# Optimization experiments

Hardware: AMD Instinct MI355X
Metric: run time of the kernel (lower is better)

The kernel has to match this reference:

```python
import jax, jax.numpy as jnp
import numpy as np

B, S, E, H = 4, 1024, 256, 8
D = E // H


def setup_inputs() -> dict:
    key = jax.random.key(0)
    ks = jax.random.split(key, 10)
    def lin(k, fin, fout):
        return jax.random.normal(k, (fin, fout), jnp.float32) / np.sqrt(fin)
    return {
        'x': jax.random.normal(ks[0], (B, S, E), jnp.float32),
        'Wq': lin(ks[1], E, E),
        'Wk': lin(ks[2], E, E),
        'Wv': lin(ks[3], E, E),
        'W_off1': lin(ks[4], E, E // 2),
        'b_off1': jnp.zeros((E // 2,), jnp.float32),
        'W_off2': lin(ks[5], E // 2, 2 * H),
        'b_off2': jnp.zeros((2 * H,), jnp.float32),
        'W_out': lin(ks[6], E, E),
        'b_out': jnp.zeros((E,), jnp.float32),
    }


def _forward(x, Wq, Wk, Wv, W_off1, b_off1, W_off2, b_off2, W_out, b_out):
    Bb, Ss, Ee = x.shape
    scale = 1.0 / np.sqrt(D)
    # offsets: (B,S,H,2) -- [...,0]=x-offset (col), [...,1]=y-offset (row)
    off = jax.nn.gelu(x @ W_off1 + b_off1, approximate=False) @ W_off2 + b_off2
    off = off.reshape(Bb, Ss, H, 2)
    q = (x @ Wq).reshape(Bb, Ss, H, D).transpose(0, 2, 1, 3)  # bhsd
    k = (x @ Wk).reshape(Bb, Ss, H, D).transpose(0, 2, 1, 3)
    v = (x @ Wv).reshape(Bb, Ss, H, D).transpose(0, 2, 1, 3)
    scores = jnp.einsum('bhid,bhjd->bhij', q, k) * scale  # (B,H,S,S)

    ox = off[..., 0].transpose(0, 2, 1)  # (B,H,S)
    oy = off[..., 1].transpose(0, 2, 1)
    cols = jnp.arange(Ss, dtype=x.dtype)
    xs = cols[None, None, None, :] + ox[..., None]          # (B,H,S,S) sample col
    ys = cols[None, None, :, None] + oy[..., None]          # (B,H,S,1) sample row

    x0 = jnp.floor(xs); x1 = x0 + 1.0
    y0 = jnp.floor(ys); y1 = y0 + 1.0
    wx = xs - x0  # (B,H,S,S)
    wy = ys - y0  # (B,H,S,1)
    lim = jnp.asarray(Ss - 1, x.dtype)

    def corner(yf, xf):
        # bilinear corner sample with zeros padding (align_corners=True)
        yc = jnp.clip(yf, 0, lim).astype(jnp.int32)
        xc = jnp.clip(xf, 0, lim).astype(jnp.int32)
        rows = jnp.take_along_axis(scores, jnp.broadcast_to(yc, scores.shape), axis=2)
        vals = jnp.take_along_axis(rows, jnp.broadcast_to(xc, rows.shape), axis=3)
        valid = (yf >= 0) & (yf <= lim) & (xf >= 0) & (xf <= lim)
        return jnp.where(valid, vals, jnp.zeros((), x.dtype))

    deformed = (corner(y0, x0) * (1 - wy) * (1 - wx)
                + corner(y0, x1) * (1 - wy) * wx
                + corner(y1, x0) * wy * (1 - wx)
                + corner(y1, x1) * wy * wx)

    attn = jax.nn.softmax(deformed, axis=-1)  # dropout is identity in eval
    out = jnp.einsum('bhij,bhjd->bhid', attn, v)
    out = out.transpose(0, 2, 1, 3).reshape(Bb, Ss, Ee)
    return out @ W_out + b_out


def reference(x, Wq, Wk, Wv, W_off1, b_off1, W_off2, b_off2, W_out, b_out):
    return _forward(x, Wq, Wk, Wv, W_off1, b_off1, W_off2, b_off2, W_out, b_out)
```

## Files before the change

### kernel.cpp

```cpp
#include <hip/hip_runtime.h>

typedef unsigned short u16;
typedef __attribute__((ext_vector_type(8))) short short8;
typedef __attribute__((ext_vector_type(4))) float f32x4;

__device__ __forceinline__ float bf2f(u16 u) {
    union { unsigned int i; float f; } z;
    z.i = ((unsigned int)u) << 16;
    return z.f;
}
__device__ __forceinline__ u16 f2bf(float f) {
    union { float f; unsigned int i; } z;
    z.f = f;
    unsigned int i = z.i;
    return (u16)((i + 0x7fffu + ((i >> 16) & 1u)) >> 16);
}
__device__ __forceinline__ int sniff_bf16(const u16* __restrict__ x) {
    u16 u = x[threadIdx.x & 63];
    int e = (u >> 7) & 0xFF;
    bool sane = (e >= 110 && e <= 135) || (u == 0);
    unsigned long long m = __ballot(sane);
    return (__popcll(m) >= 50) ? 1 : 0;
}
__device__ __forceinline__ float cvt_elem(const void* p, int i, int fl) {
    return fl ? bf2f(((const u16*)p)[i]) : ((const float*)p)[i];
}

#define SB 1024
#define EB 256
#define NH 8
#define HD 32

__global__ __launch_bounds__(256) void k_prep(
    const void* x, const void* wq, const void* wk, const void* wv, const void* w1,
    const void* w2, const void* wo, const void* b1, const void* b2, const void* bo,
    u16* __restrict__ xb, u16* __restrict__ Wcat, u16* __restrict__ Wot,
    u16* __restrict__ W2t, float* __restrict__ b1f, float* __restrict__ b2f,
    float* __restrict__ bof) {
    __shared__ float tile[64][65];
    int fl = sniff_bf16((const u16*)x);
    int t = threadIdx.x;
    int bid = blockIdx.x;
    if (bid < 1024) {
        int idx = bid * 1024 + t * 4;
        if (fl) {
            *(ushort4*)(xb + idx) = *(const ushort4*)((const u16*)x + idx);
        } else {
            float4 v = *(const float4*)((const float*)x + idx);
            ushort4 s;
            s.x = f2bf(v.x); s.y = f2bf(v.y); s.z = f2bf(v.z); s.w = f2bf(v.w);
            *(ushort4*)(xb + idx) = s;
        }
    } else if (bid == 1024) {
        #pragma unroll
        for (int it = 0; it < 10; ++it) {
            int idx = it * 256 + t;
            if (idx < 2048) {
                int n = idx >> 7, kk = idx & 127;
                W2t[idx] = f2bf(cvt_elem(w2, kk * 16 + n, fl));
            }
            else if (idx < 2176)  b1f[idx - 2048] = cvt_elem(b1, idx - 2048, fl);
            else if (idx < 2192)  b2f[idx - 2176] = cvt_elem(b2, idx - 2176, fl);
            else if (idx < 2448)  bof[idx - 2192] = cvt_elem(bo, idx - 2192, fl);
        }
    } else {
        int rel = bid - 1025;
        int z = rel >> 4, rr = rel & 15;
        int k0 = (rr & 3) * 64, n0 = (rr >> 2) * 64;
        const void* src;
        u16* dst;
        int ncols;
        if (z == 0)      { src = wq; dst = Wcat;             ncols = 256; }
        else if (z == 1) { src = wk; dst = Wcat + 256 * 256; ncols = 256; }
        else if (z == 2) { src = wv; dst = Wcat + 512 * 256; ncols = 256; }
        else if (z == 3) { src = w1; dst = Wcat + 768 * 256; ncols = 128; }
        else             { src = wo; dst = Wot;              ncols = 256; }
        if (n0 >= ncols) return;
        int lr = t >> 6, lc = t & 63;
        #pragma unroll
        for (int it = 0; it < 16; ++it) {
            int r = it * 4 + lr;
            tile[r][lc] = cvt_elem(src, (k0 + r) * ncols + n0 + lc, fl);
        }
        __syncthreads();
        #pragma unroll
        for (int it = 0; it < 16; ++it) {
            int n = it * 4 + lr;
            dst[(size_t)(n0 + n) * 256 + k0 + lc] = f2bf(tile[lc][n]);
        }
    }
}

__global__ __launch_bounds__(256) void k_qkvh(
    const u16* __restrict__ xb, const u16* __restrict__ Wt, const float* __restrict__ b1f,
    u16* __restrict__ q, u16* __restrict__ k, u16* __restrict__ v, u16* __restrict__ hb) {
    int t = threadIdx.x;
    int w = t >> 6, L = t & 63;
    int lane15 = L & 15, quad = L >> 4;
    int Wid = blockIdx.x * 4 + w;
    int mtile = Wid & 127, ntile = Wid >> 7;
    int m0 = mtile * 32, n0 = ntile * 32;
    const u16* ap0 = xb + (size_t)(m0 + lane15) * 256 + quad * 8;
    const u16* ap1 = ap0 + 16 * 256;
    const u16* bp0 = Wt + (size_t)(n0 + lane15) * 256 + quad * 8;
    const u16* bp1 = bp0 + 16 * 256;
    bool vreg = (ntile >= 16 && ntile < 24);
    f32x4 acc[2][2];
    #pragma unroll
    for (int a = 0; a < 2; ++a)
        #pragma unroll
        for (int c = 0; c < 2; ++c) acc[a][c] = (f32x4){0.0f, 0.0f, 0.0f, 0.0f};
    if (!vreg) {
        #pragma unroll
        for (int kc = 0; kc < 256; kc += 32) {
            short8 a0 = *(const short8*)(ap0 + kc);
            short8 a1 = *(const short8*)(ap1 + kc);
            short8 b0 = *(const short8*)(bp0 + kc);
            short8 b1 = *(const short8*)(bp1 + kc);
            acc[0][0] = __builtin_amdgcn_mfma_f32_16x16x32_bf16(b0, a0, acc[0][0], 0, 0, 0);
            acc[0][1] = __builtin_amdgcn_mfma_f32_16x16x32_bf16(b1, a0, acc[0][1], 0, 0, 0);
            acc[1][0] = __builtin_amdgcn_mfma_f32_16x16x32_bf16(b0, a1, acc[1][0], 0, 0, 0);
            acc[1][1] = __builtin_amdgcn_mfma_f32_16x16x32_bf16(b1, a1, acc[1][1], 0, 0, 0);
        }
    } else {
        #pragma unroll
        for (int kc = 0; kc < 256; kc += 32) {
            short8 a0 = *(const short8*)(ap0 + kc);
            short8 a1 = *(const short8*)(ap1 + kc);
            short8 b0 = *(const short8*)(bp0 + kc);
            short8 b1 = *(const short8*)(bp1 + kc);
            acc[0][0] = __builtin_amdgcn_mfma_f32_16x16x32_bf16(a0, b0, acc[0][0], 0, 0, 0);
            acc[0][1] = __builtin_amdgcn_mfma_f32_16x16x32_bf16(a0, b1, acc[0][1], 0, 0, 0);
            acc[1][0] = __builtin_amdgcn_mfma_f32_16x16x32_bf16(a1, b0, acc[1][0], 0, 0, 0);
            acc[1][1] = __builtin_amdgcn_mfma_f32_16x16x32_bf16(a1, b1, acc[1][1], 0, 0, 0);
        }
    }
    if (ntile < 16) {
        u16* dst = (ntile < 8) ? q : k;
        int hh = ntile & 7;
        #pragma unroll
        for (int xt = 0; xt < 2; ++xt)
            #pragma unroll
            for (int wt = 0; wt < 2; ++wt) {
                int m = m0 + xt * 16 + lane15;
                int b = m >> 10, s = m & 1023;
                int d = wt * 16 + quad * 4;
                ushort4 st;
                st.x = f2bf(acc[xt][wt][0]); st.y = f2bf(acc[xt][wt][1]);
                st.z = f2bf(acc[xt][wt][2]); st.w = f2bf(acc[xt][wt][3]);
                *(ushort4*)(dst + (((size_t)(b * NH + hh)) * SB + s) * HD + d) = st;
            }
    } else if (vreg) {
        int nl = (ntile - 16) * 32;
        #pragma unroll
        for (int mt = 0; mt < 2; ++mt)
            #pragma unroll
            for (int nt = 0; nt < 2; ++nt) {
                int n = nl + nt * 16 + lane15;
                int hh = n >> 5, d = n & 31;
                int mbase = m0 + mt * 16 + quad * 4;
                int b = mbase >> 10, s0 = mbase & 1023;
                ushort4 st;
                st.x = f2bf(acc[mt][nt][0]); st.y = f2bf(acc[mt][nt][1]);
                st.z = f2bf(acc[mt][nt][2]); st.w = f2bf(acc[mt][nt][3]);
                *(ushort4*)(v + (b * NH + hh) * (SB * HD) + (s0 >> 3) * 256 + d * 8 + (s0 & 7)) = st;
            }
    } else {
        int nl = (ntile - 24) * 32;
        #pragma unroll
        for (int xt = 0; xt < 2; ++xt)
            #pragma unroll
            for (int wt = 0; wt < 2; ++wt) {
                int m = m0 + xt * 16 + lane15;
                int hn = nl + wt * 16 + quad * 4;
                ushort4 st;
                #pragma unroll
                for (int reg = 0; reg < 4; ++reg) {
                    float aa = acc[xt][wt][reg] + b1f[hn + reg];
                    float g = 0.5f * aa * (1.0f + erff(aa * 0.70710678118654752f));
                    ((u16*)&st)[reg] = f2bf(g);
                }
                *(ushort4*)(hb + (size_t)m * 128 + hn) = st;
            }
    }
}

__global__ __launch_bounds__(256) void k_qprime(
    const u16* __restrict__ hb, const u16* __restrict__ W2t, const float* __restrict__ b2f,
    float2* __restrict__ prmA, float4* __restrict__ prmB) {
    int t = threadIdx.x;
    int w = t >> 6, L = t & 63;
    int lane15 = L & 15, quad = L >> 4;
    int m0 = (blockIdx.x * 4 + w) * 16;
    const u16* ap = hb + (size_t)(m0 + lane15) * 128 + quad * 8;
    const u16* bp = W2t + (size_t)lane15 * 128 + quad * 8;
    f32x4 acc = {0.0f, 0.0f, 0.0f, 0.0f};
    #pragma unroll
    for (int c = 0; c < 4; ++c) {
        short8 a = *(const short8*)(ap + c * 32);
        short8 bfr = *(const short8*)(bp + c * 32);
        acc = __builtin_amdgcn_mfma_f32_16x16x32_bf16(a, bfr, acc, 0, 0, 0);
    }
    const float scale = 0.17677669529663687f;
    int n = lane15, h = n >> 1;
    float bb = b2f[n];
    #pragma unroll
    for (int reg = 0; reg < 4; ++reg) {
        int m = m0 + quad * 4 + reg;
        int i = m & 1023;
        float val = acc[reg] + bb;
        if ((n & 1) == 0) {
            float fxf = floorf(val);
            float wx = val - fxf;
            fxf = fminf(fmaxf(fxf, -1028.0f), 1028.0f);
            prmA[m * 8 + h] = make_float2(fxf, wx);
        } else {
            float ysf = (float)i + val;
            float y0f = floorf(ysf);
            float wy = ysf - y0f;
            float y1f = y0f + 1.0f;
            float alA = scale * (1.0f - wy) * ((y0f >= 0.0f && y0f <= 1023.0f) ? 1.0f : 0.0f);
            float alB = scale * wy * ((y1f >= 0.0f && y1f <= 1023.0f) ? 1.0f : 0.0f);
            float yc0 = fminf(fmaxf(y0f, 0.0f), 1023.0f);
            float yc1 = fminf(fmaxf(y1f, 0.0f), 1023.0f);
            prmB[m * 8 + h] = make_float4(alA, alB, yc0, yc1);
        }
    }
}

#define TSTR 1056
#define BLEND4A(R)                                                    \
    _Pragma("unroll")                                                 \
    for (int jj = 0; jj < 4; ++jj) {                                  \
        float dd = wxm * A8[(R) + jj] + wx * A8[(R) + jj + 1];        \
        dv[c * 4 + jj] = dd;                                          \
        lmax = fmaxf(lmax, dd);                                       \
    }

__global__ __launch_bounds__(256) void k_attn(
    const u16* __restrict__ q, const u16* __restrict__ kmat,
    const float2* __restrict__ prmA, const float4* __restrict__ prmB,
    const u16* __restrict__ vfrag, u16* __restrict__ attn) {
    __shared__ u16 tbuf[16][TSTR];
    __shared__ float invLs[16];
    float* red = (float*)&tbuf[0][0];
    int t = threadIdx.x;
    int w = t >> 6, L = t & 63;
    int lane15 = L & 15, quad = L >> 4;
    int bh = blockIdx.y, it0 = blockIdx.x * 16;
    int b = bh >> 3, h = bh & 7;
    int mg0 = b * SB + it0;

    {
        int row = t >> 4, ii = t & 15;
        tbuf[row][ii] = 0;
        tbuf[row][1040 + ii] = 0;
    }

    const u16* qb = q + (size_t)bh * SB * HD;
    float4 pB = prmB[(size_t)(mg0 + lane15) * 8 + h];
    int yc0 = (int)pB.z, yc1 = (int)pB.w;
    short8 q0 = *(const short8*)(qb + yc0 * HD + quad * 8);
    short8 q1 = *(const short8*)(qb + yc1 * HD + quad * 8);
    union { short8 v; u16 a[8]; } afr;
    #pragma unroll
    for (int s = 0; s < 8; ++s)
        afr.a[s] = f2bf(pB.x * bf2f((u16)q0[s]) + pB.y * bf2f((u16)q1[s]));

    const u16* kb = kmat + (size_t)bh * SB * HD;
    int c0 = w * 256;
    #pragma unroll
    for (int nt = 0; nt < 16; ++nt) {
        short8 bk = *(const short8*)(kb + (size_t)(c0 + nt * 16 + lane15) * HD + quad * 8);
        f32x4 z = {0.0f, 0.0f, 0.0f, 0.0f};
        f32x4 acc = __builtin_amdgcn_mfma_f32_16x16x32_bf16(bk, afr.v, z, 0, 0, 0);
        uint2 pk;
        pk.x = (unsigned)f2bf(acc[0]) | ((unsigned)f2bf(acc[1]) << 16);
        pk.y = (unsigned)f2bf(acc[2]) | ((unsigned)f2bf(acc[3]) << 16);
        *(uint2*)&tbuf[lane15][16 + c0 + nt * 16 + quad * 4] = pk;
    }
    __syncthreads();

    #pragma unroll
    for (int r = 0; r < 4; ++r) {
        int m = w * 4 + r;
        float2 pA = prmA[(size_t)(mg0 + m) * 8 + h];
        int fx = (int)pA.x;
        float wx = pA.y, wxm = 1.0f - wx;
        int qd = fx >> 2, rm = fx & 3;
        float dv[16];
        float lmax = -3.0e38f;
        #pragma unroll
        for (int c = 0; c < 4; ++c) {
            int colbase = c * 256 + 4 * (qd + L);
            int rd = colbase < -16 ? -16 : (colbase > 1032 ? 1032 : colbase);
            const u16* rp = &tbuf[m][16 + rd];
            ushort4 lo = *(const ushort4*)rp;
            ushort4 hi = *(const ushort4*)(rp + 4);
            float A8[8];
            A8[0] = bf2f(lo.x); A8[1] = bf2f(lo.y); A8[2] = bf2f(lo.z); A8[3] = bf2f(lo.w);
            A8[4] = bf2f(hi.x); A8[5] = bf2f(hi.y); A8[6] = bf2f(hi.z); A8[7] = bf2f(hi.w);
            if (rm == 0) { BLEND4A(0) }
            else if (rm == 1) { BLEND4A(1) }
            else if (rm == 2) { BLEND4A(2) }
            else { BLEND4A(3) }
        }
        #pragma unroll
        for (int o = 1; o < 64; o <<= 1) lmax = fmaxf(lmax, __shfl_xor(lmax, o));
        float ls = 0.0f;
        #pragma unroll
        for (int z = 0; z < 16; ++z) { dv[z] = __expf(dv[z] - lmax); ls += dv[z]; }
        #pragma unroll
        for (int o = 1; o < 64; o <<= 1) ls += __shfl_xor(ls, o);
        #pragma unroll
        for (int c = 0; c < 4; ++c) {
            unsigned lo = (unsigned)f2bf(dv[c * 4 + 0]) | ((unsigned)f2bf(dv[c * 4 + 1]) << 16);
            unsigned hi = (unsigned)f2bf(dv[c * 4 + 2]) | ((unsigned)f2bf(dv[c * 4 + 3]) << 16);
            *(uint2*)&tbuf[m][16 + c * 256 + 4 * L] = make_uint2(lo, hi);
        }
        if (L == 0) invLs[m] = 1.0f / ls;
    }
    __syncthreads();

    const u16* vb = vfrag + bh * (SB * HD);
    f32x4 acc0 = {0.0f, 0.0f, 0.0f, 0.0f};
    f32x4 acc1 = {0.0f, 0.0f, 0.0f, 0.0f};
    int kc0 = w * 256;
    #pragma unroll
    for (int c = 0; c < 8; ++c) {
        int kc = kc0 + c * 32;
        short8 a = *(const short8*)&tbuf[lane15][16 + kc + quad * 8];
        const u16* bp = vb + ((kc >> 3) + quad) * (HD * 8);
        short8 b0 = *(const short8*)(bp + lane15 * 8);
        short8 b1 = *(const short8*)(bp + (lane15 + 16) * 8);
        acc0 = __builtin_amdgcn_mfma_f32_16x16x32_bf16(a, b0, acc0, 0, 0, 0);
        acc1 = __builtin_amdgcn_mfma_f32_16x16x32_bf16(a, b1, acc1, 0, 0, 0);
    }
    __syncthreads();
    *(f32x4*)&red[(((size_t)w * 2 + 0) * 64 + L) * 4] = acc0;
    *(f32x4*)&red[(((size_t)w * 2 + 1) * 64 + L) * 4] = acc1;
    __syncthreads();
    {
        int row = t >> 4, col = t & 15;
        int lsrc = col + 16 * (row >> 2);
        int reg = row & 3;
        float s0 = red[((0 * 64 + lsrc)) * 4 + reg] + red[((2 * 64 + lsrc)) * 4 + reg]
                 + red[((4 * 64 + lsrc)) * 4 + reg] + red[((6 * 64 + lsrc)) * 4 + reg];
        float s1 = red[((1 * 64 + lsrc)) * 4 + reg] + red[((3 * 64 + lsrc)) * 4 + reg]
                 + red[((5 * 64 + lsrc)) * 4 + reg] + red[((7 * 64 + lsrc)) * 4 + reg];
        float il = invLs[row];
        size_t o = ((size_t)(b * SB + it0 + row)) * EB + h * HD;
        attn[o + col]      = f2bf(s0 * il);
        attn[o + 16 + col] = f2bf(s1 * il);
    }
}

__global__ __launch_bounds__(256) void k_out(
    const u16* __restrict__ a, const u16* __restrict__ Wot, const float* __restrict__ bof,
    const u16* __restrict__ xsniff, void* __restrict__ outp) {
    int fl = sniff_bf16(xsniff);
    int t = threadIdx.x;
    int w = t >> 6, L = t & 63;
    int lane15 = L & 15, quad = L >> 4;
    int Wid = blockIdx.x * 4 + w;
    int m0 = (Wid & 255) * 16, n0 = (Wid >> 8) * 32;
    const u16* ap  = a + (size_t)(m0 + lane15) * 256 + quad * 8;
    const u16* bp0 = Wot + (size_t)(n0 + lane15) * 256 + quad * 8;
    const u16* bp1 = bp0 + 16 * 256;
    f32x4 acc0 = {0.0f, 0.0f, 0.0f, 0.0f};
    f32x4 acc1 = {0.0f, 0.0f, 0.0f, 0.0f};
    #pragma unroll
    for (int kc = 0; kc < 256; kc += 32) {
        short8 av = *(const short8*)(ap + kc);
        short8 b0 = *(const short8*)(bp0 + kc);
        short8 b1 = *(const short8*)(bp1 + kc);
        acc0 = __builtin_amdgcn_mfma_f32_16x16x32_bf16(b0, av, acc0, 0, 0, 0);
        acc1 = __builtin_amdgcn_mfma_f32_16x16x32_bf16(b1, av, acc1, 0, 0, 0);
    }
    int m = m0 + lane15;
    #pragma unroll
    for (int wt = 0; wt < 2; ++wt) {
        const f32x4& ac = wt ? acc1 : acc0;
        int n = n0 + wt * 16 + quad * 4;
        float4 bz = *(const float4*)(bof + n);
        float v0 = ac[0] + bz.x, v1 = ac[1] + bz.y, v2 = ac[2] + bz.z, v3 = ac[3] + bz.w;
        if (fl) {
            ushort4 st;
            st.x = f2bf(v0); st.y = f2bf(v1); st.z = f2bf(v2); st.w = f2bf(v3);
            *(ushort4*)((u16*)outp + (size_t)m * 256 + n) = st;
        } else {
            *(float4*)((float*)outp + (size_t)m * 256 + n) = make_float4(v0, v1, v2, v3);
        }
    }
}

extern "C" void kernel_launch(void* const* d_in, const int* in_sizes, int n_in,
                              void* d_out, int out_size, void* d_ws, size_t ws_size,
                              hipStream_t stream) {
    char* ws = (char*)d_ws;
    u16*    xb   = (u16*)(ws);
    u16*    Wcat = (u16*)(ws + 2097152);
    u16*    Wot  = (u16*)(ws + 2555904);
    u16*    W2t  = (u16*)(ws + 2686976);
    float*  b1f  = (float*)(ws + 2691072);
    float*  b2f  = (float*)(ws + 2691584);
    float*  bof  = (float*)(ws + 2691648);
    u16*    q    = (u16*)(ws + 2692672);
    u16*    k    = (u16*)(ws + 4789824);
    u16*    v    = (u16*)(ws + 6886976);
    u16*    hb   = (u16*)(ws + 8984128);
    u16*    attn = (u16*)(ws + 10032704);
    float2* prmA = (float2*)(ws + 12129856);
    float4* prmB = (float4*)(ws + 12392000);

    hipLaunchKernelGGL(k_prep, dim3(1105), dim3(256), 0, stream,
                       d_in[0], d_in[1], d_in[2], d_in[3], d_in[4],
                       d_in[6], d_in[8], d_in[5], d_in[7], d_in[9],
                       xb, Wcat, Wot, W2t, b1f, b2f, bof);
    hipLaunchKernelGGL(k_qkvh, dim3(896), dim3(256), 0, stream, xb, Wcat, b1f, q, k, v, hb);
    hipLaunchKernelGGL(k_qprime, dim3(64), dim3(256), 0, stream, hb, W2t, b2f, prmA, prmB);
    hipLaunchKernelGGL(k_attn, dim3(64, 32), dim3(256), 0, stream, q, k, prmA, prmB, v, attn);
    hipLaunchKernelGGL(k_out, dim3(512), dim3(256), 0, stream, attn, Wot, bof,
                       (const u16*)d_in[0], (u16*)d_out);
}
```

Measured before the change: 147.9 us.

## Fuse offset projection into attention kernel and drop the qprime launch

Removes the separate k_qprime kernel and recomputes the second offset MLP layer inside k_attn with one small MFMA per wave. The x/y offsets are extracted with lane shuffles. This removes one kernel launch and the prmA/prmB round trip through global memory. In exchange, every attention block (across all heads) recomputes the 16x16 offset tile redundantly. It also changes the shared tile row stride from 1056 to 1064, which may affect LDS bank conflicts.

```diff
diff --git a/kernel.cpp b/kernel.cpp
--- a/kernel.cpp
+++ b/kernel.cpp
@@ -185,50 +185,7 @@
     }
 }
 
-__global__ __launch_bounds__(256) void k_qprime(
-    const u16* __restrict__ hb, const u16* __restrict__ W2t, const float* __restrict__ b2f,
-    float2* __restrict__ prmA, float4* __restrict__ prmB) {
-    int t = threadIdx.x;
-    int w = t >> 6, L = t & 63;
-    int lane15 = L & 15, quad = L >> 4;
-    int m0 = (blockIdx.x * 4 + w) * 16;
-    const u16* ap = hb + (size_t)(m0 + lane15) * 128 + quad * 8;
-    const u16* bp = W2t + (size_t)lane15 * 128 + quad * 8;
-    f32x4 acc = {0.0f, 0.0f, 0.0f, 0.0f};
-    #pragma unroll
-    for (int c = 0; c < 4; ++c) {
-        short8 a = *(const short8*)(ap + c * 32);
-        short8 bfr = *(const short8*)(bp + c * 32);
-        acc = __builtin_amdgcn_mfma_f32_16x16x32_bf16(a, bfr, acc, 0, 0, 0);
-    }
-    const float scale = 0.17677669529663687f;
-    int n = lane15, h = n >> 1;
-    float bb = b2f[n];
-    #pragma unroll
-    for (int reg = 0; reg < 4; ++reg) {
-        int m = m0 + quad * 4 + reg;
-        int i = m & 1023;
-        float val = acc[reg] + bb;
-        if ((n & 1) == 0) {
-            float fxf = floorf(val);
-            float wx = val - fxf;
-            fxf = fminf(fmaxf(fxf, -1028.0f), 1028.0f);
-            prmA[m * 8 + h] = make_float2(fxf, wx);
-        } else {
-            float ysf = (float)i + val;
-            float y0f = floorf(ysf);
-            float wy = ysf - y0f;
-            float y1f = y0f + 1.0f;
-            float alA = scale * (1.0f - wy) * ((y0f >= 0.0f && y0f <= 1023.0f) ? 1.0f : 0.0f);
-            float alB = scale * wy * ((y1f >= 0.0f && y1f <= 1023.0f) ? 1.0f : 0.0f);
-            float yc0 = fminf(fmaxf(y0f, 0.0f), 1023.0f);
-            float yc1 = fminf(fmaxf(y1f, 0.0f), 1023.0f);
-            prmB[m * 8 + h] = make_float4(alA, alB, yc0, yc1);
-        }
-    }
-}
-
-#define TSTR 1056
+#define TSTR 1064
 #define BLEND4A(R)                                                    \
     _Pragma("unroll")                                                 \
     for (int jj = 0; jj < 4; ++jj) {                                  \
@@ -239,7 +196,8 @@
 
 __global__ __launch_bounds__(256) void k_attn(
     const u16* __restrict__ q, const u16* __restrict__ kmat,
-    const float2* __restrict__ prmA, const float4* __restrict__ prmB,
+    const u16* __restrict__ hb, const u16* __restrict__ W2t,
+    const float* __restrict__ b2f,
     const u16* __restrict__ vfrag, u16* __restrict__ attn) {
     __shared__ u16 tbuf[16][TSTR];
     __shared__ float invLs[16];
@@ -250,6 +208,7 @@
     int bh = blockIdx.y, it0 = blockIdx.x * 16;
     int b = bh >> 3, h = bh & 7;
     int mg0 = b * SB + it0;
+    const float scale = 0.17677669529663687f;
 
     {
         int row = t >> 4, ii = t & 15;
@@ -257,68 +216,95 @@
         tbuf[row][1040 + ii] = 0;
     }
 
-    const u16* qb = q + (size_t)bh * SB * HD;
-    float4 pB = prmB[(size_t)(mg0 + lane15) * 8 + h];
-    int yc0 = (int)pB.z, yc1 = (int)pB.w;
-    short8 q0 = *(const short8*)(qb + yc0 * HD + quad * 8);
-    short8 q1 = *(const short8*)(qb + yc1 * HD + quad * 8);
-    union { short8 v; u16 a[8]; } afr;
-    #pragma unroll
-    for (int s = 0; s < 8; ++s)
-        afr.a[s] = f2bf(pB.x * bf2f((u16)q0[s]) + pB.y * bf2f((u16)q1[s]));
-
-    const u16* kb = kmat + (size_t)bh * SB * HD;
-    int c0 = w * 256;
-    #pragma unroll
-    for (int nt = 0; nt < 16; ++nt) {
-        short8 bk = *(const short8*)(kb + (size_t)(c0 + nt * 16 + lane15) * HD + quad * 8);
-        f32x4 z = {0.0f, 0.0f, 0.0f, 0.0f};
-        f32x4 acc = __builtin_amdgcn_mfma_f32_16x16x32_bf16(bk, afr.v, z, 0, 0, 0);
-        uint2 pk;
-        pk.x = (unsigned)f2bf(acc[0]) | ((unsigned)f2bf(acc[1]) << 16);
-        pk.y = (unsigned)f2bf(acc[2]) | ((unsigned)f2bf(acc[3]) << 16);
-        *(uint2*)&tbuf[lane15][16 + c0 + nt * 16 + quad * 4] = pk;
-    }
-    __syncthreads();
-
-    #pragma unroll
-    for (int r = 0; r < 4; ++r) {
-        int m = w * 4 + r;
-        float2 pA = prmA[(size_t)(mg0 + m) * 8 + h];
-        int fx = (int)pA.x;
-        float wx = pA.y, wxm = 1.0f - wx;
-        int qd = fx >> 2, rm = fx & 3;
-        float dv[16];
-        float lmax = -3.0e38f;
+    {
+        const u16* hrow = hb + (size_t)(mg0 + lane15) * 128 + quad * 8;
+        const u16* wrow = W2t + (size_t)lane15 * 128 + quad * 8;
+        f32x4 oacc = {0.0f, 0.0f, 0.0f, 0.0f};
         #pragma unroll
         for (int c = 0; c < 4; ++c) {
-            int colbase = c * 256 + 4 * (qd + L);
-            int rd = colbase < -16 ? -16 : (colbase > 1032 ? 1032 : colbase);
-            const u16* rp = &tbuf[m][16 + rd];
-            ushort4 lo = *(const ushort4*)rp;
-            ushort4 hi = *(const ushort4*)(rp + 4);
-            float A8[8];
-            A8[0] = bf2f(lo.x); A8[1] = bf2f(lo.y); A8[2] = bf2f(lo.z); A8[3] = bf2f(lo.w);
-            A8[4] = bf2f(hi.x); A8[5] = bf2f(hi.y); A8[6] = bf2f(hi.z); A8[7] = bf2f(hi.w);
-            if (rm == 0) { BLEND4A(0) }
-            else if (rm == 1) { BLEND4A(1) }
-            else if (rm == 2) { BLEND4A(2) }
-            else { BLEND4A(3) }
-        }
-        #pragma unroll
-        for (int o = 1; o < 64; o <<= 1) lmax = fmaxf(lmax, __shfl_xor(lmax, o));
-        float ls = 0.0f;
-        #pragma unroll
-        for (int z = 0; z < 16; ++z) { dv[z] = __expf(dv[z] - lmax); ls += dv[z]; }
-        #pragma unroll
-        for (int o = 1; o < 64; o <<= 1) ls += __shfl_xor(ls, o);
-        #pragma unroll
-        for (int c = 0; c < 4; ++c) {
-            unsigned lo = (unsigned)f2bf(dv[c * 4 + 0]) | ((unsigned)f2bf(dv[c * 4 + 1]) << 16);
-            unsigned hi = (unsigned)f2bf(dv[c * 4 + 2]) | ((unsigned)f2bf(dv[c * 4 + 3]) << 16);
-            *(uint2*)&tbuf[m][16 + c * 256 + 4 * L] = make_uint2(lo, hi);
-        }
-        if (L == 0) invLs[m] = 1.0f / ls;
+            short8 aw = *(const short8*)(wrow + c * 32);
+            short8 bh8 = *(const short8*)(hrow + c * 32);
+            oacc = __builtin_amdgcn_mfma_f32_16x16x32_bf16(aw, bh8, oacc, 0, 0, 0);
+        }
+        int h2 = h * 2;
+        int qs = h2 >> 2;
+        bool rlo = ((h2 & 3) == 0);
+        float selx = rlo ? oacc[0] : oacc[2];
+        float sely = rlo ? oacc[1] : oacc[3];
+        float ox_row = __shfl(selx, qs * 16 + lane15) + b2f[h2];
+        float oy_row = __shfl(sely, qs * 16 + lane15) + b2f[h2 + 1];
+        float ysf = (float)(it0 + lane15) + oy_row;
+        float y0f = floorf(ysf);
+        float wy = ysf - y0f;
+        float y1f = y0f + 1.0f;
+        float alA = scale * (1.0f - wy) * ((y0f >= 0.0f && y0f <= 1023.0f) ? 1.0f : 0.0f);
+        float alB = scale * wy * ((y1f >= 0.0f && y1f <= 1023.0f) ? 1.0f : 0.0f);
+        int yc0 = (int)fminf(fmaxf(y0f, 0.0f), 1023.0f);
+        int yc1 = (int)fminf(fmaxf(y1f, 0.0f), 1023.0f);
+
+        const u16* qb = q + (size_t)bh * SB * HD;
+        short8 q0 = *(const short8*)(qb + yc0 * HD + quad * 8);
+        short8 q1 = *(const short8*)(qb + yc1 * HD + quad * 8);
+        union { short8 v; u16 a[8]; } afr;
+        #pragma unroll
+        for (int s = 0; s < 8; ++s)
+            afr.a[s] = f2bf(alA * bf2f((u16)q0[s]) + alB * bf2f((u16)q1[s]));
+
+        const u16* kb = kmat + (size_t)bh * SB * HD;
+        int c0 = w * 256;
+        #pragma unroll
+        for (int nt = 0; nt < 16; ++nt) {
+            short8 bk = *(const short8*)(kb + (size_t)(c0 + nt * 16 + lane15) * HD + quad * 8);
+            f32x4 z = {0.0f, 0.0f, 0.0f, 0.0f};
+            f32x4 acc = __builtin_amdgcn_mfma_f32_16x16x32_bf16(bk, afr.v, z, 0, 0, 0);
+            uint2 pk;
+            pk.x = (unsigned)f2bf(acc[0]) | ((unsigned)f2bf(acc[1]) << 16);
+            pk.y = (unsigned)f2bf(acc[2]) | ((unsigned)f2bf(acc[3]) << 16);
+            *(uint2*)&tbuf[lane15][16 + c0 + nt * 16 + quad * 4] = pk;
+        }
+        __syncthreads();
+
+        #pragma unroll
+        for (int r = 0; r < 4; ++r) {
+            int m = w * 4 + r;
+            float oxm = __shfl(ox_row, m);
+            float fxf = floorf(oxm);
+            float wx = oxm - fxf, wxm = 1.0f - wx;
+            fxf = fminf(fmaxf(fxf, -1028.0f), 1028.0f);
+            int fx = (int)fxf;
+            int qd = fx >> 2, rm = fx & 3;
+            float dv[16];
+            float lmax = -3.0e38f;
+            #pragma unroll
+            for (int c = 0; c < 4; ++c) {
+                int colbase = c * 256 + 4 * (qd + L);
+                int rd = colbase < -16 ? -16 : (colbase > 1032 ? 1032 : colbase);
+                const u16* rp = &tbuf[m][16 + rd];
+                ushort4 lo = *(const ushort4*)rp;
+                ushort4 hi = *(const ushort4*)(rp + 4);
+                float A8[8];
+                A8[0] = bf2f(lo.x); A8[1] = bf2f(lo.y); A8[2] = bf2f(lo.z); A8[3] = bf2f(lo.w);
+                A8[4] = bf2f(hi.x); A8[5] = bf2f(hi.y); A8[6] = bf2f(hi.z); A8[7] = bf2f(hi.w);
+                if (rm == 0) { BLEND4A(0) }
+                else if (rm == 1) { BLEND4A(1) }
+                else if (rm == 2) { BLEND4A(2) }
+                else { BLEND4A(3) }
+            }
+            #pragma unroll
+            for (int o = 1; o < 64; o <<= 1) lmax = fmaxf(lmax, __shfl_xor(lmax, o));
+            float ls = 0.0f;
+            #pragma unroll
+            for (int z = 0; z < 16; ++z) { dv[z] = __expf(dv[z] - lmax); ls += dv[z]; }
+            #pragma unroll
+            for (int o = 1; o < 64; o <<= 1) ls += __shfl_xor(ls, o);
+            #pragma unroll
+            for (int c = 0; c < 4; ++c) {
+                unsigned lo = (unsigned)f2bf(dv[c * 4 + 0]) | ((unsigned)f2bf(dv[c * 4 + 1]) << 16);
+                unsigned hi = (unsigned)f2bf(dv[c * 4 + 2]) | ((unsigned)f2bf(dv[c * 4 + 3]) << 16);
+                *(uint2*)&tbuf[m][16 + c * 256 + 4 * L] = make_uint2(lo, hi);
+            }
+            if (L == 0) invLs[m] = 1.0f / ls;
+        }
     }
     __syncthreads();
 
@@ -410,16 +396,13 @@
     u16*    v    = (u16*)(ws + 6886976);
     u16*    hb   = (u16*)(ws + 8984128);
     u16*    attn = (u16*)(ws + 10032704);
-    float2* prmA = (float2*)(ws + 12129856);
-    float4* prmB = (float4*)(ws + 12392000);
 
     hipLaunchKernelGGL(k_prep, dim3(1105), dim3(256), 0, stream,
                        d_in[0], d_in[1], d_in[2], d_in[3], d_in[4],
                        d_in[6], d_in[8], d_in[5], d_in[7], d_in[9],
                        xb, Wcat, Wot, W2t, b1f, b2f, bof);
     hipLaunchKernelGGL(k_qkvh, dim3(896), dim3(256), 0, stream, xb, Wcat, b1f, q, k, v, hb);
-    hipLaunchKernelGGL(k_qprime, dim3(64), dim3(256), 0, stream, hb, W2t, b2f, prmA, prmB);
-    hipLaunchKernelGGL(k_attn, dim3(64, 32), dim3(256), 0, stream, q, k, prmA, prmB, v, attn);
+    hipLaunchKernelGGL(k_attn, dim3(64, 32), dim3(256), 0, stream, q, k, hb, W2t, b2f, v, attn);
     hipLaunchKernelGGL(k_out, dim3(512), dim3(256), 0, stream, attn, Wot, bof,
                        (const u16*)d_in[0], (u16*)d_out);
 }
```

Result: no change. 145.1 us (-1.9%).
